# Kernel tuning notes

Measured on AMD Instinct MI355X. Metric: run time of the kernel, lower is better.

## Reference

```python
import jax, jax.numpy as jnp
import numpy as np

PILLAR_SIZE = 0.075
PC_RANGE = (-54.0, -54.0, -5.0, 54.0, 54.0, 3.0)
H = round((PC_RANGE[4] - PC_RANGE[1]) / PILLAR_SIZE)  # 1440
W = round((PC_RANGE[3] - PC_RANGE[0]) / PILLAR_SIZE)  # 1440
X_OFFSET = PILLAR_SIZE / 2.0 + PC_RANGE[0]
Y_OFFSET = PILLAR_SIZE / 2.0 + PC_RANGE[1]
BATCH = 4
N_PER_BATCH = 500_000
C_FEAT = 16


def setup_inputs() -> dict:
    key = jax.random.key(0)
    k1, k2, k3 = jax.random.split(key, 3)
    N = BATCH * N_PER_BATCH
    # integer pillar-grid coordinates (x, y) of each point
    pts_xy = jax.random.randint(k1, (N, 2), 0, W, dtype=jnp.int32)
    pts_batch_cnt = jnp.full((BATCH,), N_PER_BATCH, dtype=jnp.int32)
    feats = jax.random.normal(k2, (N, C_FEAT), dtype=jnp.float32)
    # first two channels are the absolute xy coordinates of the points
    base = jnp.array([PC_RANGE[0], PC_RANGE[1]], dtype=jnp.float32)
    xy = (pts_xy.astype(jnp.float32) * PILLAR_SIZE + base
          + jax.random.uniform(k3, (N, 2), dtype=jnp.float32) * PILLAR_SIZE)
    feats = feats.at[:, :2].set(xy)
    return {"pts_xy": pts_xy, "pts_batch_cnt": pts_batch_cnt, "pts_features": feats}


def reference(pts_xy, pts_batch_cnt, pts_features):
    batch = pts_batch_cnt.shape[0]
    N = pts_xy.shape[0]
    # batch index of each point from the per-batch counts
    batch_idx = jnp.repeat(jnp.arange(batch, dtype=jnp.int32), pts_batch_cnt,
                           total_repeat_length=N)
    x = pts_xy[:, 0].astype(jnp.int32)
    y = pts_xy[:, 1].astype(jnp.int32)
    # flat pillar id per point: (b, y, x) -> b*H*W + y*W + x  (== point_pillar_index)
    flat = (batch_idx * H + y) * W + x
    # scatter: mark occupied pillars
    mask = jnp.zeros((batch * H * W,), dtype=bool).at[flat].set(True)
    # cumsum compaction: rank of each occupied pillar (row-major order), -1 elsewhere
    csum = jnp.cumsum(mask.astype(jnp.int32))
    positions = jnp.where(mask, csum - 1, -1)
    # indices of active pillars (sorted flat order == compaction order)
    active = jnp.nonzero(mask)[0]                      # (P,) data-dependent size
    b = (active // (H * W)).astype(jnp.int32)
    rem = active % (H * W)
    hy = (rem // W).astype(jnp.int32)
    wx = (rem % W).astype(jnp.int32)
    pillar_indices = jnp.stack([b, hy, wx], axis=1)    # (P, 3) [batch, y, x]
    # compact pillar index per point
    point_pillar_indices = positions[flat]             # (N,)
    # pillar centers in world coords, gathered back to points
    pillar_centers = jnp.stack([wx.astype(jnp.float32) * PILLAR_SIZE + X_OFFSET,
                                hy.astype(jnp.float32) * PILLAR_SIZE + Y_OFFSET],
                               axis=1)                 # (P, 2)
    point_pillar_centers = pts_features[:, :2] - pillar_centers[point_pillar_indices]
    point_pillar_features = jnp.concatenate([point_pillar_centers, pts_features], axis=1)
    return pillar_indices, point_pillar_indices, point_pillar_features
```

## Files before the change

kernel.cpp:

```cpp
#include <hip/hip_runtime.h>

namespace {

constexpr int   HG  = 1440;
constexpr int   WG  = 1440;
constexpr int   HWG = HG * WG;
constexpr float PIL = 0.075f;
constexpr float XOFF = (float)(0.075 / 2.0 - 54.0);
constexpr float YOFF = XOFF;

constexpr int SCAN_T    = 256;
constexpr int SCAN_WPT  = 4;
constexpr int SCAN_CHUNK = SCAN_T * SCAN_WPT;

__global__ __launch_bounds__(256) void scatter_k(
    const int* __restrict__ xy, const int* __restrict__ cnt, int batch, int N,
    unsigned int* __restrict__ bits)
{
    int i = blockIdx.x * 256 + threadIdx.x;
    if (i >= N) return;
    int2 p = reinterpret_cast<const int2*>(xy)[i];
    int b = 0, acc = 0;
    for (int k = 0; k < batch - 1; ++k) { acc += cnt[k]; b += (i >= acc) ? 1 : 0; }
    int flat = (b * HG + p.y) * WG + p.x;
    atomicOr(&bits[flat >> 5], 1u << (flat & 31));
}

__global__ __launch_bounds__(SCAN_T) void scan_a(
    const unsigned int* __restrict__ bits, int nwords,
    unsigned int* __restrict__ bsums)
{
    int t = threadIdx.x;
    int base = blockIdx.x * SCAN_CHUNK + t * SCAN_WPT;
    unsigned int s = 0;
    if (base + SCAN_WPT <= nwords) {
        uint4 q = *reinterpret_cast<const uint4*>(bits + base);
        s = __popc(q.x) + __popc(q.y) + __popc(q.z) + __popc(q.w);
    } else {
        for (int k = 0; k < SCAN_WPT; ++k)
            if (base + k < nwords) s += __popc(bits[base + k]);
    }
#pragma unroll
    for (int d = 32; d > 0; d >>= 1) s += __shfl_down(s, d);
    __shared__ unsigned int red[SCAN_T / 64];
    if ((t & 63) == 0) red[t >> 6] = s;
    __syncthreads();
    if (t == 0) {
        unsigned int tot = 0;
        for (int w = 0; w < SCAN_T / 64; ++w) tot += red[w];
        bsums[blockIdx.x] = tot;
    }
}

__global__ __launch_bounds__(SCAN_T) void scan_b(unsigned int* bsums, int nb)
{
    int t = threadIdx.x;
    unsigned int v = (t < nb) ? bsums[t] : 0u;
    unsigned int x = v;
#pragma unroll
    for (int d = 1; d < 64; d <<= 1) {
        unsigned int y = __shfl_up(x, d);
        if ((t & 63) >= d) x += y;
    }
    __shared__ unsigned int ws[SCAN_T / 64];
    if ((t & 63) == 63) ws[t >> 6] = x;
    __syncthreads();
    unsigned int off = 0;
    for (int w = 0; w < (t >> 6); ++w) off += ws[w];
    if (t < nb) bsums[t] = off + x - v;
}

__global__ __launch_bounds__(SCAN_T) void scan_c(
    const unsigned int* __restrict__ bits, int nwords,
    const unsigned int* __restrict__ bsums,
    unsigned int* __restrict__ wordscan,
    float* __restrict__ pillar_out)
{
    int t = threadIdx.x;
    int base = blockIdx.x * SCAN_CHUNK + t * SCAN_WPT;
    unsigned int w[SCAN_WPT];
    if (base + SCAN_WPT <= nwords) {
        uint4 q = *reinterpret_cast<const uint4*>(bits + base);
        w[0] = q.x; w[1] = q.y; w[2] = q.z; w[3] = q.w;
    } else {
        for (int k = 0; k < SCAN_WPT; ++k)
            w[k] = (base + k < nwords) ? bits[base + k] : 0u;
    }
    unsigned int s = 0;
#pragma unroll
    for (int k = 0; k < SCAN_WPT; ++k) s += __popc(w[k]);
    unsigned int x = s;
#pragma unroll
    for (int d = 1; d < 64; d <<= 1) {
        unsigned int y = __shfl_up(x, d);
        if ((t & 63) >= d) x += y;
    }
    __shared__ unsigned int ws[SCAN_T / 64];
    if ((t & 63) == 63) ws[t >> 6] = x;
    __syncthreads();
    unsigned int run = bsums[blockIdx.x] + x - s;
    for (int wv = 0; wv < (t >> 6); ++wv) run += ws[wv];
#pragma unroll
    for (int k = 0; k < SCAN_WPT; ++k) {
        int widx = base + k;
        if (widx >= nwords) break;
        wordscan[widx] = run;
        unsigned int bw = w[k];
        while (bw) {
            int bit = __builtin_ctz(bw);
            bw &= bw - 1u;
            int cell = (widx << 5) + bit;
            int bidx = cell / HWG;
            int rem  = cell - bidx * HWG;
            int hy   = rem / WG;
            int wx   = rem - hy * WG;
            float* row = pillar_out + 3ull * run;
            row[0] = (float)bidx;
            row[1] = (float)hy;
            row[2] = (float)wx;
            ++run;
        }
    }
}

constexpr int PT_T = 256;
__global__ __launch_bounds__(PT_T) void point_k(
    const int* __restrict__ xy, const int* __restrict__ cnt, int batch,
    const float* __restrict__ feats, int N,
    const unsigned int* __restrict__ bits,
    const unsigned int* __restrict__ wordscan,
    float* __restrict__ ppi_out, float* __restrict__ feat_out)
{
    __shared__ float lds[PT_T][19];
    int t = threadIdx.x;
    int blockBase = blockIdx.x * PT_T;
    int i = blockBase + t;
    int nvalid = N - blockBase; if (nvalid > PT_T) nvalid = PT_T;

    if (t < nvalid) {
        int2 p = reinterpret_cast<const int2*>(xy)[i];
        int b = 0, acc = 0;
        for (int k = 0; k < batch - 1; ++k) { acc += cnt[k]; b += (i >= acc) ? 1 : 0; }
        int flat = (b * HG + p.y) * WG + p.x;
        int widx = flat >> 5, bit = flat & 31;
        unsigned int pid = wordscan[widx] + __popc(bits[widx] & ((1u << bit) - 1u));
        ppi_out[i] = (float)pid;

        const float4* fr = reinterpret_cast<const float4*>(feats + 16ll * i);
        float4 f0 = fr[0], f1 = fr[1], f2 = fr[2], f3 = fr[3];
        float cx = (float)p.x * PIL + XOFF;
        float cy = (float)p.y * PIL + YOFF;
        lds[t][0]  = f0.x - cx;  lds[t][1]  = f0.y - cy;
        lds[t][2]  = f0.x;  lds[t][3]  = f0.y;  lds[t][4]  = f0.z;  lds[t][5]  = f0.w;
        lds[t][6]  = f1.x;  lds[t][7]  = f1.y;  lds[t][8]  = f1.z;  lds[t][9]  = f1.w;
        lds[t][10] = f2.x;  lds[t][11] = f2.y;  lds[t][12] = f2.z;  lds[t][13] = f2.w;
        lds[t][14] = f3.x;  lds[t][15] = f3.y;  lds[t][16] = f3.z;  lds[t][17] = f3.w;
    }
    __syncthreads();

    float* dst = feat_out + 18ll * blockBase;
    int total = nvalid * 18;
    for (int j = t; j < total; j += PT_T) {
        int p = j / 18;
        int c = j - p * 18;
        dst[j] = lds[p][c];
    }
}

}

extern "C" void kernel_launch(void* const* d_in, const int* in_sizes, int n_in,
                              void* d_out, int out_size, void* d_ws, size_t ws_size,
                              hipStream_t stream)
{
    const int*   xy    = (const int*)d_in[0];
    const int*   cnt   = (const int*)d_in[1];
    const float* feats = (const float*)d_in[2];

    int N     = in_sizes[0] / 2;
    int batch = in_sizes[1];
    long long ncells = (long long)batch * HWG;
    int nwords = (int)(ncells / 32);
    long long P = (out_size - 19ll * N) / 3;

    unsigned int* bits     = (unsigned int*)d_ws;
    unsigned int* wordscan = bits + nwords;
    unsigned int* bsums    = wordscan + nwords;

    float* pillar_out = (float*)d_out;
    float* ppi_out    = pillar_out + 3ll * P;
    float* feat_out   = ppi_out + N;

    hipMemsetAsync(bits, 0, (size_t)nwords * sizeof(unsigned int), stream);

    int nb_pts = (N + 255) / 256;
    scatter_k<<<nb_pts, 256, 0, stream>>>(xy, cnt, batch, N, bits);

    int nb_scan = (nwords + SCAN_CHUNK - 1) / SCAN_CHUNK;
    scan_a<<<nb_scan, SCAN_T, 0, stream>>>(bits, nwords, bsums);
    scan_b<<<1, SCAN_T, 0, stream>>>(bsums, nb_scan);
    scan_c<<<nb_scan, SCAN_T, 0, stream>>>(bits, nwords, bsums, wordscan, pillar_out);

    point_k<<<nb_pts, PT_T, 0, stream>>>(xy, cnt, batch, feats, N, bits, wordscan,
                                         ppi_out, feat_out);
}
```

Baseline: 377.4 us.

## Replace atomic bitmask scatter with bytemap and split pillar emission into per-cell kernel

Points now mark occupancy with plain byte stores into a bytemap instead of atomicOr on a packed bitmask, which removes atomic contention. The scan kernels read the bytemap (8x more memory traffic) and pack it into bits plus per-word prefix sums. Pillar rows are then written by a new one-thread-per-cell emit kernel instead of a serial ctz loop inside the scan. Point-stage loads and stores and the emit stores use nontemporal hints. The tradeoff is an extra launch and reading roughly 8 MB of bytemap twice, plus a larger memset.

```diff
diff --git a/kernel.cpp b/kernel.cpp
--- a/kernel.cpp
+++ b/kernel.cpp
@@ -1,6 +1,8 @@
 #include <hip/hip_runtime.h>
 
 namespace {
+
+typedef float f32x4 __attribute__((ext_vector_type(4)));
 
 constexpr int   HG  = 1440;
 constexpr int   WG  = 1440;
@@ -13,9 +15,17 @@
 constexpr int SCAN_WPT  = 4;
 constexpr int SCAN_CHUNK = SCAN_T * SCAN_WPT;
 
-__global__ __launch_bounds__(256) void scatter_k(
+__device__ inline unsigned nib4(unsigned u) {
+    return (u * 0x01020408u) >> 24 & 0xFu;
+}
+__device__ inline unsigned pack_word(uint4 a, uint4 b) {
+    return  nib4(a.x)        | nib4(a.y) << 4  | nib4(a.z) << 8  | nib4(a.w) << 12
+          | nib4(b.x) << 16  | nib4(b.y) << 20 | nib4(b.z) << 24 | nib4(b.w) << 28;
+}
+
+__global__ __launch_bounds__(256) void pqag_scatter(
     const int* __restrict__ xy, const int* __restrict__ cnt, int batch, int N,
-    unsigned int* __restrict__ bits)
+    unsigned char* __restrict__ bytemap)
 {
     int i = blockIdx.x * 256 + threadIdx.x;
     if (i >= N) return;
@@ -23,22 +33,26 @@
     int b = 0, acc = 0;
     for (int k = 0; k < batch - 1; ++k) { acc += cnt[k]; b += (i >= acc) ? 1 : 0; }
     int flat = (b * HG + p.y) * WG + p.x;
-    atomicOr(&bits[flat >> 5], 1u << (flat & 31));
-}
-
-__global__ __launch_bounds__(SCAN_T) void scan_a(
-    const unsigned int* __restrict__ bits, int nwords,
+    bytemap[flat] = 1;
+}
+
+__global__ __launch_bounds__(SCAN_T) void pqag_scan_a(
+    const unsigned char* __restrict__ bytemap, int nwords,
     unsigned int* __restrict__ bsums)
 {
     int t = threadIdx.x;
-    int base = blockIdx.x * SCAN_CHUNK + t * SCAN_WPT;
+    int wbase = blockIdx.x * SCAN_CHUNK + t * SCAN_WPT;
     unsigned int s = 0;
-    if (base + SCAN_WPT <= nwords) {
-        uint4 q = *reinterpret_cast<const uint4*>(bits + base);
-        s = __popc(q.x) + __popc(q.y) + __popc(q.z) + __popc(q.w);
+    if (wbase + SCAN_WPT <= nwords) {
+        const uint4* q = reinterpret_cast<const uint4*>(bytemap) + 2ll * wbase;
+#pragma unroll
+        for (int k = 0; k < 2 * SCAN_WPT; ++k) {
+            uint4 v = q[k];
+            s += __popc(v.x) + __popc(v.y) + __popc(v.z) + __popc(v.w);
+        }
     } else {
-        for (int k = 0; k < SCAN_WPT; ++k)
-            if (base + k < nwords) s += __popc(bits[base + k]);
+        for (int w = wbase; w < nwords && w < wbase + SCAN_WPT; ++w)
+            for (int j = 0; j < 32; ++j) s += bytemap[32 * w + j];
     }
 #pragma unroll
     for (int d = 32; d > 0; d >>= 1) s += __shfl_down(s, d);
@@ -52,7 +66,7 @@
     }
 }
 
-__global__ __launch_bounds__(SCAN_T) void scan_b(unsigned int* bsums, int nb)
+__global__ __launch_bounds__(SCAN_T) void pqag_scan_b(unsigned int* bsums, int nb)
 {
     int t = threadIdx.x;
     unsigned int v = (t < nb) ? bsums[t] : 0u;
@@ -70,21 +84,28 @@
     if (t < nb) bsums[t] = off + x - v;
 }
 
-__global__ __launch_bounds__(SCAN_T) void scan_c(
-    const unsigned int* __restrict__ bits, int nwords,
+__global__ __launch_bounds__(SCAN_T) void pqag_scan_c(
+    const unsigned char* __restrict__ bytemap, int nwords,
     const unsigned int* __restrict__ bsums,
-    unsigned int* __restrict__ wordscan,
-    float* __restrict__ pillar_out)
-{
-    int t = threadIdx.x;
-    int base = blockIdx.x * SCAN_CHUNK + t * SCAN_WPT;
+    unsigned int* __restrict__ bits,
+    unsigned int* __restrict__ wordscan)
+{
+    int t = threadIdx.x;
+    int wbase = blockIdx.x * SCAN_CHUNK + t * SCAN_WPT;
     unsigned int w[SCAN_WPT];
-    if (base + SCAN_WPT <= nwords) {
-        uint4 q = *reinterpret_cast<const uint4*>(bits + base);
-        w[0] = q.x; w[1] = q.y; w[2] = q.z; w[3] = q.w;
+    if (wbase + SCAN_WPT <= nwords) {
+        const uint4* q = reinterpret_cast<const uint4*>(bytemap) + 2ll * wbase;
+#pragma unroll
+        for (int k = 0; k < SCAN_WPT; ++k)
+            w[k] = pack_word(q[2 * k], q[2 * k + 1]);
     } else {
-        for (int k = 0; k < SCAN_WPT; ++k)
-            w[k] = (base + k < nwords) ? bits[base + k] : 0u;
+        for (int k = 0; k < SCAN_WPT; ++k) {
+            unsigned int wv = 0;
+            if (wbase + k < nwords)
+                for (int j = 0; j < 32; ++j)
+                    wv |= (unsigned)(bytemap[32 * (wbase + k) + j]) << j;
+            w[k] = wv;
+        }
     }
     unsigned int s = 0;
 #pragma unroll
@@ -102,29 +123,38 @@
     for (int wv = 0; wv < (t >> 6); ++wv) run += ws[wv];
 #pragma unroll
     for (int k = 0; k < SCAN_WPT; ++k) {
-        int widx = base + k;
+        int widx = wbase + k;
         if (widx >= nwords) break;
+        bits[widx]     = w[k];
         wordscan[widx] = run;
-        unsigned int bw = w[k];
-        while (bw) {
-            int bit = __builtin_ctz(bw);
-            bw &= bw - 1u;
-            int cell = (widx << 5) + bit;
-            int bidx = cell / HWG;
-            int rem  = cell - bidx * HWG;
-            int hy   = rem / WG;
-            int wx   = rem - hy * WG;
-            float* row = pillar_out + 3ull * run;
-            row[0] = (float)bidx;
-            row[1] = (float)hy;
-            row[2] = (float)wx;
-            ++run;
-        }
+        run += __popc(w[k]);
+    }
+}
+
+__global__ __launch_bounds__(256) void pqag_emit(
+    const unsigned int* __restrict__ bits,
+    const unsigned int* __restrict__ wordscan, int ncells,
+    float* __restrict__ pillar_out)
+{
+    int cell = blockIdx.x * 256 + threadIdx.x;
+    if (cell >= ncells) return;
+    unsigned int word = bits[cell >> 5];
+    int bit = cell & 31;
+    if ((word >> bit) & 1u) {
+        unsigned int pid = wordscan[cell >> 5] + __popc(word & ((1u << bit) - 1u));
+        int bidx = cell / HWG;
+        int rem  = cell - bidx * HWG;
+        int hy   = rem / WG;
+        int wx   = rem - hy * WG;
+        float* row = pillar_out + 3ull * pid;
+        __builtin_nontemporal_store((float)bidx, row + 0);
+        __builtin_nontemporal_store((float)hy,   row + 1);
+        __builtin_nontemporal_store((float)wx,   row + 2);
     }
 }
 
 constexpr int PT_T = 256;
-__global__ __launch_bounds__(PT_T) void point_k(
+__global__ __launch_bounds__(PT_T) void pqag_point(
     const int* __restrict__ xy, const int* __restrict__ cnt, int batch,
     const float* __restrict__ feats, int N,
     const unsigned int* __restrict__ bits,
@@ -144,10 +174,13 @@
         int flat = (b * HG + p.y) * WG + p.x;
         int widx = flat >> 5, bit = flat & 31;
         unsigned int pid = wordscan[widx] + __popc(bits[widx] & ((1u << bit) - 1u));
-        ppi_out[i] = (float)pid;
-
-        const float4* fr = reinterpret_cast<const float4*>(feats + 16ll * i);
-        float4 f0 = fr[0], f1 = fr[1], f2 = fr[2], f3 = fr[3];
+        __builtin_nontemporal_store((float)pid, ppi_out + i);
+
+        const f32x4* fr = reinterpret_cast<const f32x4*>(feats + 16ll * i);
+        f32x4 f0 = __builtin_nontemporal_load(fr + 0);
+        f32x4 f1 = __builtin_nontemporal_load(fr + 1);
+        f32x4 f2 = __builtin_nontemporal_load(fr + 2);
+        f32x4 f3 = __builtin_nontemporal_load(fr + 3);
         float cx = (float)p.x * PIL + XOFF;
         float cy = (float)p.y * PIL + YOFF;
         lds[t][0]  = f0.x - cx;  lds[t][1]  = f0.y - cy;
@@ -163,7 +196,7 @@
     for (int j = t; j < total; j += PT_T) {
         int p = j / 18;
         int c = j - p * 18;
-        dst[j] = lds[p][c];
+        __builtin_nontemporal_store(lds[p][c], dst + j);
     }
 }
 
@@ -179,28 +212,32 @@
 
     int N     = in_sizes[0] / 2;
     int batch = in_sizes[1];
-    long long ncells = (long long)batch * HWG;
-    int nwords = (int)(ncells / 32);
+    int ncells = batch * HWG;
+    int nwords = ncells / 32;
     long long P = (out_size - 19ll * N) / 3;
 
-    unsigned int* bits     = (unsigned int*)d_ws;
-    unsigned int* wordscan = bits + nwords;
-    unsigned int* bsums    = wordscan + nwords;
+    unsigned char* bytemap  = (unsigned char*)d_ws;
+    unsigned int*  bits     = (unsigned int*)(bytemap + ncells);
+    unsigned int*  wordscan = bits + nwords;
+    unsigned int*  bsums    = wordscan + nwords;
 
     float* pillar_out = (float*)d_out;
     float* ppi_out    = pillar_out + 3ll * P;
     float* feat_out   = ppi_out + N;
 
-    hipMemsetAsync(bits, 0, (size_t)nwords * sizeof(unsigned int), stream);
+    (void)hipMemsetAsync(bytemap, 0, (size_t)ncells, stream);
 
     int nb_pts = (N + 255) / 256;
-    scatter_k<<<nb_pts, 256, 0, stream>>>(xy, cnt, batch, N, bits);
+    pqag_scatter<<<nb_pts, 256, 0, stream>>>(xy, cnt, batch, N, bytemap);
 
     int nb_scan = (nwords + SCAN_CHUNK - 1) / SCAN_CHUNK;
-    scan_a<<<nb_scan, SCAN_T, 0, stream>>>(bits, nwords, bsums);
-    scan_b<<<1, SCAN_T, 0, stream>>>(bsums, nb_scan);
-    scan_c<<<nb_scan, SCAN_T, 0, stream>>>(bits, nwords, bsums, wordscan, pillar_out);
-
-    point_k<<<nb_pts, PT_T, 0, stream>>>(xy, cnt, batch, feats, N, bits, wordscan,
-                                         ppi_out, feat_out);
-}
+    pqag_scan_a<<<nb_scan, SCAN_T, 0, stream>>>(bytemap, nwords, bsums);
+    pqag_scan_b<<<1, SCAN_T, 0, stream>>>(bsums, nb_scan);
+    pqag_scan_c<<<nb_scan, SCAN_T, 0, stream>>>(bytemap, nwords, bsums, bits, wordscan);
+
+    int nb_emit = (ncells + 255) / 256;
+    pqag_emit<<<nb_emit, 256, 0, stream>>>(bits, wordscan, ncells, pillar_out);
+
+    pqag_point<<<nb_pts, PT_T, 0, stream>>>(xy, cnt, batch, feats, N, bits, wordscan,
+                                            ppi_out, feat_out);
+}
```

Result: faster. 357.7 us (-5.2%).
